# Kernel optimization log

Hardware: AMD Instinct MI355X
Metric: run time of the kernel (lower is better)

Reference implementation:

```python
import jax, jax.numpy as jnp
import numpy as np

EPS = 1e-12  # matches F.normalize eps
K = 256      # prototype_num


def _l2norm(v, axis=-1):
    n = jnp.linalg.norm(v, axis=axis, keepdims=True)
    return v / jnp.maximum(n, EPS)


def setup_inputs() -> dict:
    key = jax.random.key(0)
    k1, k2, k3, k4 = jax.random.split(key, 4)
    B, N, D = 8, 16384, 768
    x = jax.random.normal(k1, (B, N, D), dtype=jnp.float32)
    prototypes = jax.random.normal(k2, (K, D), dtype=jnp.float32)
    W = jax.random.normal(k3, (D, D), dtype=jnp.float32) * (1.0 / np.sqrt(D))
    b = jax.random.normal(k4, (D,), dtype=jnp.float32) * 0.01
    return {"x": x, "prototypes": prototypes, "W": W, "b": b}


def reference(x, prototypes, W, b):
    # cosine similarity: (B,N,D) x (K,D) -> (B,N,K)
    sim = jnp.einsum('bnd,kd->bnk', _l2norm(x), _l2norm(prototypes))
    prob = jax.nn.softmax(sim, axis=-1)
    # weighted prototype mixture, scaled by 1/prototype_num
    x_proto = jnp.einsum('bnk,kd->bnd', prob, prototypes) / K
    # final linear projection (PyTorch Linear: x @ W.T + b)
    return jnp.einsum('bnd,ed->bne', x_proto, W) + b
```

## Files before the change

kernel.cpp:

```cpp
#include <hip/hip_runtime.h>
#include <hip/hip_bf16.h>

typedef unsigned short u16;
typedef __attribute__((ext_vector_type(8))) short bf16x8;
typedef __attribute__((ext_vector_type(4))) float f32x4;

__device__ __forceinline__ u16 f32_to_bf16(float f) {
  unsigned int x = __float_as_uint(f);
  x += 0x7fffu + ((x >> 16) & 1u);
  return (u16)(x >> 16);
}

__global__ __launch_bounds__(256) void prep_pn_kernel(const float* __restrict__ P,
                                                      u16* __restrict__ pn_sw) {
  const int n = blockIdx.x;
  const int t = threadIdx.x;
  float v0 = P[n * 768 + t];
  float v1 = P[n * 768 + t + 256];
  float v2 = P[n * 768 + t + 512];
  float ss = v0 * v0 + v1 * v1 + v2 * v2;
#pragma unroll
  for (int m = 1; m < 64; m <<= 1) ss += __shfl_xor(ss, m, 64);
  __shared__ float wsum[4];
  if ((t & 63) == 0) wsum[t >> 6] = ss;
  __syncthreads();
  const float inv = 1.0f / fmaxf(sqrtf(wsum[0] + wsum[1] + wsum[2] + wsum[3]), 1e-12f);
  float vv[3] = {v0, v1, v2};
#pragma unroll
  for (int i = 0; i < 3; ++i) {
    int d = t + i * 256;
    int c = d >> 5, q = (d >> 3) & 3, j = d & 7;
    pn_sw[c * 8192 + n * 32 + q * 8 + j] = f32_to_bf16(vv[i] * inv);
  }
}

__global__ __launch_bounds__(256) void prep_pw_kernel(const float* __restrict__ P,
                                                      const float* __restrict__ W,
                                                      u16* __restrict__ pw_sw) {
  const int e0 = blockIdx.x * 4;
  const int t = threadIdx.x;
  __shared__ float Wl[4 * 768];
#pragma unroll
  for (int i = 0; i < 12; ++i) Wl[t + i * 256] = W[e0 * 768 + t + i * 256];
  __syncthreads();
  const float* prow = P + t * 768;
  float a0 = 0.f, a1 = 0.f, a2 = 0.f, a3 = 0.f;
  for (int d = 0; d < 768; d += 4) {
    float4 p = *(const float4*)(prow + d);
    a0 += p.x * Wl[d] + p.y * Wl[d + 1] + p.z * Wl[d + 2] + p.w * Wl[d + 3];
    a1 += p.x * Wl[768 + d] + p.y * Wl[768 + d + 1] + p.z * Wl[768 + d + 2] + p.w * Wl[768 + d + 3];
    a2 += p.x * Wl[1536 + d] + p.y * Wl[1536 + d + 1] + p.z * Wl[1536 + d + 2] + p.w * Wl[1536 + d + 3];
    a3 += p.x * Wl[2304 + d] + p.y * Wl[2304 + d + 1] + p.z * Wl[2304 + d + 2] + p.w * Wl[2304 + d + 3];
  }
  const int s = t >> 5, q = (t >> 3) & 3, j8 = t & 7;
  const float sc = 1.0f / 256.0f;
  float av[4] = {a0, a1, a2, a3};
#pragma unroll
  for (int j = 0; j < 4; ++j)
    pw_sw[((s * 768 + e0 + j) * 4 + q) * 8 + j8] = f32_to_bf16(av[j] * sc);
}

__global__ __launch_bounds__(256, 3) void fused_kernel(const float* __restrict__ x,
                                                       const u16* __restrict__ pn_sw,
                                                       const u16* __restrict__ pw_sw,
                                                       const float* __restrict__ bias,
                                                       float* __restrict__ out) {
  __shared__ u16 xn[32 * 776];
  __shared__ float invn[32];
  __shared__ float rmax[4][32];
  __shared__ float rsum[4][32];
  u16* probL = xn;

  const int t = threadIdx.x;
  const int w = t >> 6;
  const int lane = t & 63;
  const int r = lane & 15, q = lane >> 4;
  const long row0 = (long)blockIdx.x * 32;

  {
    const int row = t >> 3, s8 = t & 7;
    const float4* xr = (const float4*)(x + (row0 + row) * 768);
    float ss = 0.f;
#pragma unroll
    for (int j = 0; j < 24; ++j) {
      float4 f = xr[s8 + j * 8];
      ss += f.x * f.x + f.y * f.y + f.z * f.z + f.w * f.w;
      ushort4 u;
      u.x = f32_to_bf16(f.x); u.y = f32_to_bf16(f.y);
      u.z = f32_to_bf16(f.z); u.w = f32_to_bf16(f.w);
      *(ushort4*)&xn[row * 776 + (s8 + j * 8) * 4] = u;
    }
    ss += __shfl_xor(ss, 1, 8);
    ss += __shfl_xor(ss, 2, 8);
    ss += __shfl_xor(ss, 4, 8);
    if (s8 == 0) invn[row] = 1.0f / fmaxf(sqrtf(ss), 1e-12f);
  }

  const u16* bP = pn_sw + (w * 64 + r) * 32 + q * 8;
  bf16x8 cb0 = *(const bf16x8*)(bP);
  bf16x8 cb1 = *(const bf16x8*)(bP + 512);
  bf16x8 cb2 = *(const bf16x8*)(bP + 1024);
  bf16x8 cb3 = *(const bf16x8*)(bP + 1536);
  __syncthreads();

  f32x4 accA[4], accB[4];
#pragma unroll
  for (int ct = 0; ct < 4; ++ct) {
    accA[ct] = f32x4{0.f, 0.f, 0.f, 0.f};
    accB[ct] = f32x4{0.f, 0.f, 0.f, 0.f};
  }
  const u16* aP0 = &xn[r * 776 + q * 8];
  const u16* aP1 = &xn[(16 + r) * 776 + q * 8];
#pragma unroll 4
  for (int c = 0; c < 23; ++c) {
    bf16x8 nb0 = *(const bf16x8*)(bP + (c + 1) * 8192);
    bf16x8 nb1 = *(const bf16x8*)(bP + (c + 1) * 8192 + 512);
    bf16x8 nb2 = *(const bf16x8*)(bP + (c + 1) * 8192 + 1024);
    bf16x8 nb3 = *(const bf16x8*)(bP + (c + 1) * 8192 + 1536);
    bf16x8 a0 = *(const bf16x8*)(aP0 + c * 32);
    bf16x8 a1 = *(const bf16x8*)(aP1 + c * 32);
    accA[0] = __builtin_amdgcn_mfma_f32_16x16x32_bf16(a0, cb0, accA[0], 0, 0, 0);
    accB[0] = __builtin_amdgcn_mfma_f32_16x16x32_bf16(a1, cb0, accB[0], 0, 0, 0);
    accA[1] = __builtin_amdgcn_mfma_f32_16x16x32_bf16(a0, cb1, accA[1], 0, 0, 0);
    accB[1] = __builtin_amdgcn_mfma_f32_16x16x32_bf16(a1, cb1, accB[1], 0, 0, 0);
    accA[2] = __builtin_amdgcn_mfma_f32_16x16x32_bf16(a0, cb2, accA[2], 0, 0, 0);
    accB[2] = __builtin_amdgcn_mfma_f32_16x16x32_bf16(a1, cb2, accB[2], 0, 0, 0);
    accA[3] = __builtin_amdgcn_mfma_f32_16x16x32_bf16(a0, cb3, accA[3], 0, 0, 0);
    accB[3] = __builtin_amdgcn_mfma_f32_16x16x32_bf16(a1, cb3, accB[3], 0, 0, 0);
    cb0 = nb0; cb1 = nb1; cb2 = nb2; cb3 = nb3;
  }
  {
    bf16x8 a0 = *(const bf16x8*)(aP0 + 23 * 32);
    bf16x8 a1 = *(const bf16x8*)(aP1 + 23 * 32);
    accA[0] = __builtin_amdgcn_mfma_f32_16x16x32_bf16(a0, cb0, accA[0], 0, 0, 0);
    accB[0] = __builtin_amdgcn_mfma_f32_16x16x32_bf16(a1, cb0, accB[0], 0, 0, 0);
    accA[1] = __builtin_amdgcn_mfma_f32_16x16x32_bf16(a0, cb1, accA[1], 0, 0, 0);
    accB[1] = __builtin_amdgcn_mfma_f32_16x16x32_bf16(a1, cb1, accB[1], 0, 0, 0);
    accA[2] = __builtin_amdgcn_mfma_f32_16x16x32_bf16(a0, cb2, accA[2], 0, 0, 0);
    accB[2] = __builtin_amdgcn_mfma_f32_16x16x32_bf16(a1, cb2, accB[2], 0, 0, 0);
    accA[3] = __builtin_amdgcn_mfma_f32_16x16x32_bf16(a0, cb3, accA[3], 0, 0, 0);
    accB[3] = __builtin_amdgcn_mfma_f32_16x16x32_bf16(a1, cb3, accB[3], 0, 0, 0);
  }

  const int rbA = q * 4;
#pragma unroll
  for (int i = 0; i < 4; ++i) {
    float mA = fmaxf(fmaxf(accA[0][i], accA[1][i]), fmaxf(accA[2][i], accA[3][i]));
    float mB = fmaxf(fmaxf(accB[0][i], accB[1][i]), fmaxf(accB[2][i], accB[3][i]));
    mA = fmaxf(mA, __shfl_xor(mA, 1, 16));
    mA = fmaxf(mA, __shfl_xor(mA, 2, 16));
    mA = fmaxf(mA, __shfl_xor(mA, 4, 16));
    mA = fmaxf(mA, __shfl_xor(mA, 8, 16));
    mB = fmaxf(mB, __shfl_xor(mB, 1, 16));
    mB = fmaxf(mB, __shfl_xor(mB, 2, 16));
    mB = fmaxf(mB, __shfl_xor(mB, 4, 16));
    mB = fmaxf(mB, __shfl_xor(mB, 8, 16));
    if (r == 0) {
      rmax[w][rbA + i] = mA;
      rmax[w][16 + rbA + i] = mB;
    }
  }
  __syncthreads();
#pragma unroll
  for (int i = 0; i < 4; ++i) {
    const int rowA = rbA + i, rowB = 16 + rbA + i;
    const float mxA = fmaxf(fmaxf(rmax[0][rowA], rmax[1][rowA]), fmaxf(rmax[2][rowA], rmax[3][rowA]));
    const float mxB = fmaxf(fmaxf(rmax[0][rowB], rmax[1][rowB]), fmaxf(rmax[2][rowB], rmax[3][rowB]));
    const float ivA = invn[rowA], ivB = invn[rowB];
    float sA = 0.f, sB = 0.f;
#pragma unroll
    for (int ct = 0; ct < 4; ++ct) {
      float eA = __expf((accA[ct][i] - mxA) * ivA);
      float eB = __expf((accB[ct][i] - mxB) * ivB);
      accA[ct][i] = eA; accB[ct][i] = eB;
      sA += eA; sB += eB;
    }
    sA += __shfl_xor(sA, 1, 16);
    sA += __shfl_xor(sA, 2, 16);
    sA += __shfl_xor(sA, 4, 16);
    sA += __shfl_xor(sA, 8, 16);
    sB += __shfl_xor(sB, 1, 16);
    sB += __shfl_xor(sB, 2, 16);
    sB += __shfl_xor(sB, 4, 16);
    sB += __shfl_xor(sB, 8, 16);
    if (r == 0) {
      rsum[w][rowA] = sA;
      rsum[w][rowB] = sB;
    }
  }
  __syncthreads();
#pragma unroll
  for (int i = 0; i < 4; ++i) {
    const int rowA = rbA + i, rowB = 16 + rbA + i;
    const float isA = 1.0f / (rsum[0][rowA] + rsum[1][rowA] + rsum[2][rowA] + rsum[3][rowA]);
    const float isB = 1.0f / (rsum[0][rowB] + rsum[1][rowB] + rsum[2][rowB] + rsum[3][rowB]);
#pragma unroll
    for (int ct = 0; ct < 4; ++ct) {
      probL[rowA * 264 + w * 64 + ct * 16 + r] = f32_to_bf16(accA[ct][i] * isA);
      probL[rowB * 264 + w * 64 + ct * 16 + r] = f32_to_bf16(accB[ct][i] * isB);
    }
  }
  __syncthreads();

  const u16* aQ0 = &probL[r * 264 + q * 8];
  const u16* aQ1 = &probL[(16 + r) * 264 + q * 8];
  for (int pass = 0; pass < 3; ++pass) {
    const int e0 = w * 192 + pass * 64;
    bf16x8 bb0 = *(const bf16x8*)(pw_sw + ((e0 + r) * 4 + q) * 8);
    bf16x8 bb1 = *(const bf16x8*)(pw_sw + ((e0 + 16 + r) * 4 + q) * 8);
    bf16x8 bb2 = *(const bf16x8*)(pw_sw + ((e0 + 32 + r) * 4 + q) * 8);
    bf16x8 bb3 = *(const bf16x8*)(pw_sw + ((e0 + 48 + r) * 4 + q) * 8);
    f32x4 o0[4], o1[4];
#pragma unroll
    for (int ct = 0; ct < 4; ++ct) {
      o0[ct] = f32x4{0.f, 0.f, 0.f, 0.f};
      o1[ct] = f32x4{0.f, 0.f, 0.f, 0.f};
    }
#pragma unroll
    for (int s = 0; s < 8; ++s) {
      bf16x8 a0 = *(const bf16x8*)(aQ0 + s * 32);
      bf16x8 a1 = *(const bf16x8*)(aQ1 + s * 32);
      bf16x8 n0, n1, n2, n3;
      if (s < 7) {
        n0 = *(const bf16x8*)(pw_sw + (((s + 1) * 768 + e0 + r) * 4 + q) * 8);
        n1 = *(const bf16x8*)(pw_sw + (((s + 1) * 768 + e0 + 16 + r) * 4 + q) * 8);
        n2 = *(const bf16x8*)(pw_sw + (((s + 1) * 768 + e0 + 32 + r) * 4 + q) * 8);
        n3 = *(const bf16x8*)(pw_sw + (((s + 1) * 768 + e0 + 48 + r) * 4 + q) * 8);
      }
      o0[0] = __builtin_amdgcn_mfma_f32_16x16x32_bf16(a0, bb0, o0[0], 0, 0, 0);
      o1[0] = __builtin_amdgcn_mfma_f32_16x16x32_bf16(a1, bb0, o1[0], 0, 0, 0);
      o0[1] = __builtin_amdgcn_mfma_f32_16x16x32_bf16(a0, bb1, o0[1], 0, 0, 0);
      o1[1] = __builtin_amdgcn_mfma_f32_16x16x32_bf16(a1, bb1, o1[1], 0, 0, 0);
      o0[2] = __builtin_amdgcn_mfma_f32_16x16x32_bf16(a0, bb2, o0[2], 0, 0, 0);
      o1[2] = __builtin_amdgcn_mfma_f32_16x16x32_bf16(a1, bb2, o1[2], 0, 0, 0);
      o0[3] = __builtin_amdgcn_mfma_f32_16x16x32_bf16(a0, bb3, o0[3], 0, 0, 0);
      o1[3] = __builtin_amdgcn_mfma_f32_16x16x32_bf16(a1, bb3, o1[3], 0, 0, 0);
      if (s < 7) { bb0 = n0; bb1 = n1; bb2 = n2; bb3 = n3; }
    }
#pragma unroll
    for (int ct = 0; ct < 4; ++ct) {
      const int e = e0 + ct * 16 + r;
      const float bv = bias[e];
#pragma unroll
      for (int i = 0; i < 4; ++i) {
        out[(row0 + q * 4 + i) * 768 + e] = o0[ct][i] + bv;
        out[(row0 + 16 + q * 4 + i) * 768 + e] = o1[ct][i] + bv;
      }
    }
  }
}

extern "C" void kernel_launch(void* const* d_in, const int* in_sizes, int n_in,
                              void* d_out, int out_size, void* d_ws, size_t ws_size,
                              hipStream_t stream) {
  const float* x = (const float*)d_in[0];
  const float* P = (const float*)d_in[1];
  const float* W = (const float*)d_in[2];
  const float* b = (const float*)d_in[3];
  float* out = (float*)d_out;

  u16* pn_sw = (u16*)d_ws;
  u16* pw_sw = (u16*)d_ws + 256 * 768;

  hipLaunchKernelGGL(prep_pn_kernel, dim3(256), dim3(256), 0, stream, P, pn_sw);
  hipLaunchKernelGGL(prep_pw_kernel, dim3(192), dim3(256), 0, stream, P, W, pw_sw);
  hipLaunchKernelGGL(fused_kernel, dim3(4096), dim3(256), 0, stream, x, pn_sw, pw_sw, b, out);
}
```

Baseline: 829.5 us.

## Load x fragments straight into registers and drop the LDS staging buffer

Each wave now reads its x rows from global memory straight into registers, one k-chunk ahead. It converts them to bf16 and accumulates the squared norm inline, instead of first staging the whole 32x768 tile in LDS as bf16. This removes the LDS tile, the staging pass and one block barrier. The smaller LDS footprint allows launch bounds to rise from 3 to 5 blocks per CU. The cost is that all four waves load and convert the same x rows, quadrupling global/L1 traffic for x and the conversion ALU work.

After: 1.261 ms. 52.0% more time.

```diff
diff --git a/kernel.cpp b/kernel.cpp
--- a/kernel.cpp
+++ b/kernel.cpp
@@ -9,6 +9,17 @@
   unsigned int x = __float_as_uint(f);
   x += 0x7fffu + ((x >> 16) & 1u);
   return (u16)(x >> 16);
+}
+
+__device__ __forceinline__ bf16x8 cvt_frag(float4 u, float4 v, float& ss) {
+  ss += u.x * u.x + u.y * u.y + u.z * u.z + u.w * u.w;
+  ss += v.x * v.x + v.y * v.y + v.z * v.z + v.w * v.w;
+  bf16x8 a;
+  a[0] = (short)f32_to_bf16(u.x); a[1] = (short)f32_to_bf16(u.y);
+  a[2] = (short)f32_to_bf16(u.z); a[3] = (short)f32_to_bf16(u.w);
+  a[4] = (short)f32_to_bf16(v.x); a[5] = (short)f32_to_bf16(v.y);
+  a[6] = (short)f32_to_bf16(v.z); a[7] = (short)f32_to_bf16(v.w);
+  return a;
 }
 
 __global__ __launch_bounds__(256) void prep_pn_kernel(const float* __restrict__ P,
@@ -60,16 +71,15 @@
     pw_sw[((s * 768 + e0 + j) * 4 + q) * 8 + j8] = f32_to_bf16(av[j] * sc);
 }
 
-__global__ __launch_bounds__(256, 3) void fused_kernel(const float* __restrict__ x,
+__global__ __launch_bounds__(256, 5) void fused_kernel(const float* __restrict__ x,
                                                        const u16* __restrict__ pn_sw,
                                                        const u16* __restrict__ pw_sw,
                                                        const float* __restrict__ bias,
                                                        float* __restrict__ out) {
-  __shared__ u16 xn[32 * 776];
+  __shared__ u16 probL[32 * 264];
   __shared__ float invn[32];
   __shared__ float rmax[4][32];
   __shared__ float rsum[4][32];
-  u16* probL = xn;
 
   const int t = threadIdx.x;
   const int w = t >> 6;
@@ -77,31 +87,18 @@
   const int r = lane & 15, q = lane >> 4;
   const long row0 = (long)blockIdx.x * 32;
 
-  {
-    const int row = t >> 3, s8 = t & 7;
-    const float4* xr = (const float4*)(x + (row0 + row) * 768);
-    float ss = 0.f;
-#pragma unroll
-    for (int j = 0; j < 24; ++j) {
-      float4 f = xr[s8 + j * 8];
-      ss += f.x * f.x + f.y * f.y + f.z * f.z + f.w * f.w;
-      ushort4 u;
-      u.x = f32_to_bf16(f.x); u.y = f32_to_bf16(f.y);
-      u.z = f32_to_bf16(f.z); u.w = f32_to_bf16(f.w);
-      *(ushort4*)&xn[row * 776 + (s8 + j * 8) * 4] = u;
-    }
-    ss += __shfl_xor(ss, 1, 8);
-    ss += __shfl_xor(ss, 2, 8);
-    ss += __shfl_xor(ss, 4, 8);
-    if (s8 == 0) invn[row] = 1.0f / fmaxf(sqrtf(ss), 1e-12f);
-  }
-
+  const float* xr0 = x + (row0 + r) * 768 + q * 8;
+  const float* xr1 = xr0 + 16 * 768;
   const u16* bP = pn_sw + (w * 64 + r) * 32 + q * 8;
+
+  float4 p0lo = *(const float4*)(xr0);
+  float4 p0hi = *(const float4*)(xr0 + 4);
+  float4 p1lo = *(const float4*)(xr1);
+  float4 p1hi = *(const float4*)(xr1 + 4);
   bf16x8 cb0 = *(const bf16x8*)(bP);
   bf16x8 cb1 = *(const bf16x8*)(bP + 512);
   bf16x8 cb2 = *(const bf16x8*)(bP + 1024);
   bf16x8 cb3 = *(const bf16x8*)(bP + 1536);
-  __syncthreads();
 
   f32x4 accA[4], accB[4];
 #pragma unroll
@@ -109,16 +106,20 @@
     accA[ct] = f32x4{0.f, 0.f, 0.f, 0.f};
     accB[ct] = f32x4{0.f, 0.f, 0.f, 0.f};
   }
-  const u16* aP0 = &xn[r * 776 + q * 8];
-  const u16* aP1 = &xn[(16 + r) * 776 + q * 8];
+  float ss0 = 0.f, ss1 = 0.f;
+
 #pragma unroll 4
   for (int c = 0; c < 23; ++c) {
+    float4 n0lo = *(const float4*)(xr0 + (c + 1) * 32);
+    float4 n0hi = *(const float4*)(xr0 + (c + 1) * 32 + 4);
+    float4 n1lo = *(const float4*)(xr1 + (c + 1) * 32);
+    float4 n1hi = *(const float4*)(xr1 + (c + 1) * 32 + 4);
     bf16x8 nb0 = *(const bf16x8*)(bP + (c + 1) * 8192);
     bf16x8 nb1 = *(const bf16x8*)(bP + (c + 1) * 8192 + 512);
     bf16x8 nb2 = *(const bf16x8*)(bP + (c + 1) * 8192 + 1024);
     bf16x8 nb3 = *(const bf16x8*)(bP + (c + 1) * 8192 + 1536);
-    bf16x8 a0 = *(const bf16x8*)(aP0 + c * 32);
-    bf16x8 a1 = *(const bf16x8*)(aP1 + c * 32);
+    bf16x8 a0 = cvt_frag(p0lo, p0hi, ss0);
+    bf16x8 a1 = cvt_frag(p1lo, p1hi, ss1);
     accA[0] = __builtin_amdgcn_mfma_f32_16x16x32_bf16(a0, cb0, accA[0], 0, 0, 0);
     accB[0] = __builtin_amdgcn_mfma_f32_16x16x32_bf16(a1, cb0, accB[0], 0, 0, 0);
     accA[1] = __builtin_amdgcn_mfma_f32_16x16x32_bf16(a0, cb1, accA[1], 0, 0, 0);
@@ -127,11 +128,12 @@
     accB[2] = __builtin_amdgcn_mfma_f32_16x16x32_bf16(a1, cb2, accB[2], 0, 0, 0);
     accA[3] = __builtin_amdgcn_mfma_f32_16x16x32_bf16(a0, cb3, accA[3], 0, 0, 0);
     accB[3] = __builtin_amdgcn_mfma_f32_16x16x32_bf16(a1, cb3, accB[3], 0, 0, 0);
+    p0lo = n0lo; p0hi = n0hi; p1lo = n1lo; p1hi = n1hi;
     cb0 = nb0; cb1 = nb1; cb2 = nb2; cb3 = nb3;
   }
   {
-    bf16x8 a0 = *(const bf16x8*)(aP0 + 23 * 32);
-    bf16x8 a1 = *(const bf16x8*)(aP1 + 23 * 32);
+    bf16x8 a0 = cvt_frag(p0lo, p0hi, ss0);
+    bf16x8 a1 = cvt_frag(p1lo, p1hi, ss1);
     accA[0] = __builtin_amdgcn_mfma_f32_16x16x32_bf16(a0, cb0, accA[0], 0, 0, 0);
     accB[0] = __builtin_amdgcn_mfma_f32_16x16x32_bf16(a1, cb0, accB[0], 0, 0, 0);
     accA[1] = __builtin_amdgcn_mfma_f32_16x16x32_bf16(a0, cb1, accA[1], 0, 0, 0);
@@ -140,6 +142,15 @@
     accB[2] = __builtin_amdgcn_mfma_f32_16x16x32_bf16(a1, cb2, accB[2], 0, 0, 0);
     accA[3] = __builtin_amdgcn_mfma_f32_16x16x32_bf16(a0, cb3, accA[3], 0, 0, 0);
     accB[3] = __builtin_amdgcn_mfma_f32_16x16x32_bf16(a1, cb3, accB[3], 0, 0, 0);
+  }
+
+  ss0 += __shfl_xor(ss0, 16, 64);
+  ss0 += __shfl_xor(ss0, 32, 64);
+  ss1 += __shfl_xor(ss1, 16, 64);
+  ss1 += __shfl_xor(ss1, 32, 64);
+  if (q == 0) {
+    invn[r] = 1.0f / fmaxf(sqrtf(ss0), 1e-12f);
+    invn[16 + r] = 1.0f / fmaxf(sqrtf(ss1), 1e-12f);
   }
 
   const int rbA = q * 4;
```
